# Kernel tuning notes

Hardware: AMD Instinct MI355X
Metric: run time of the kernel (lower is better)

The kernel has to match this reference:

```python
import jax, jax.numpy as jnp
import numpy as np

C = 1024
RANK = 8


def _layernorm(x, g, b, eps=1e-5):
    mu = jnp.mean(x, axis=-1, keepdims=True)
    var = jnp.var(x, axis=-1, keepdims=True)
    return (x - mu) * jax.lax.rsqrt(var + eps) * g + b


def setup_inputs() -> dict:
    key = jax.random.key(0)
    ks = jax.random.split(key, 10)
    B, T = 4, 4096
    x = jax.random.normal(ks[0], (B, T, C), dtype=jnp.float32)
    # parameters (match torch inits)
    W0 = jnp.eye(C, dtype=jnp.float32) * 0.1
    A_init = jax.random.normal(ks[1], (C, RANK), dtype=jnp.float32) * 0.01
    B_init = jnp.zeros((RANK, C), dtype=jnp.float32)
    log_lr = jnp.full((C,), float(np.log(0.1)), dtype=jnp.float32)
    s = 1.0 / np.sqrt(C)
    Wq = jax.random.uniform(ks[2], (C, C), minval=-s, maxval=s, dtype=jnp.float32)
    Wk = jax.random.uniform(ks[3], (C, C), minval=-s, maxval=s, dtype=jnp.float32)
    Wv = jax.random.uniform(ks[4], (C, C), minval=-s, maxval=s, dtype=jnp.float32)
    Wo = jax.random.uniform(ks[5], (C, C), minval=-s, maxval=s, dtype=jnp.float32)
    Wg = jax.random.uniform(ks[6], (C, C), minval=-s, maxval=s, dtype=jnp.float32)
    ln_g = jnp.ones((C,), dtype=jnp.float32)
    ln_b = jnp.zeros((C,), dtype=jnp.float32)
    ls_g = jnp.full((C,), 1e-4, dtype=jnp.float32)  # LayerScale gamma
    return {"x": x, "W0": W0, "A_init": A_init, "B_init": B_init,
            "log_lr": log_lr, "Wq": Wq, "Wk": Wk, "Wv": Wv, "Wo": Wo,
            "Wg": Wg, "ln_g": ln_g, "ln_b": ln_b, "ls_g": ls_g}


def reference(x, W0, A_init, B_init, log_lr, Wq, Wk, Wv, Wo, Wg, ln_g, ln_b, ls_g):
    B, T, _ = x.shape
    h = _layernorm(x, ln_g, ln_b)
    # dual-form TTT (training path: q/k/v projections, full K @ W0)
    Q = jnp.einsum('btc,dc->btd', h, Wq)
    K = jnp.einsum('btc,dc->btd', h, Wk)
    V = jnp.einsum('btc,dc->btd', h, Wv)
    lr = jnp.minimum(jnp.exp(log_lr), 1.0)  # clamp(max=1.0)
    y0 = jnp.einsum('btc,cd->btd', K, W0) + jnp.einsum('btr,rd->btd', jnp.einsum('btc,cr->btr', K, A_init), B_init)
    error = y0 - V
    loss = jnp.mean(error ** 2)
    gradient = K * error                     # [B,T,C]
    grad_cumsum = jnp.cumsum(gradient, axis=1)
    grad_shift = jnp.concatenate([jnp.zeros((B, 1, gradient.shape[-1]), gradient.dtype), grad_cumsum[:, :-1, :]], axis=1)
    correction = Q * lr[None, None, :] * grad_shift
    pos = jnp.arange(1, T + 1, dtype=correction.dtype)
    pos_scale = (1.0 / (1.0 + 0.1 * jnp.log(pos)))[None, :, None]
    out = y0 - correction * pos_scale
    # gate, out projection, layer scale, residual
    gate = jax.nn.sigmoid(jnp.einsum('btc,dc->btd', x, Wg))
    out = out * gate
    out = jnp.einsum('btc,dc->btd', out, Wo) * ls_g
    return (x + out, loss)
```

## Files before the change

### kernel.cpp

```cpp
#include <hip/hip_runtime.h>
#include <stdint.h>
#include <math.h>

typedef unsigned short u16;
typedef __attribute__((ext_vector_type(8))) short short8;
typedef __attribute__((ext_vector_type(4))) float f32x4;

__device__ __forceinline__ float bf2f(u16 u){
  union { unsigned int i; float f; } v; v.i = ((unsigned int)u) << 16; return v.f;
}
__device__ __forceinline__ u16 f2bf(float f){
  union { float f; unsigned int i; } v; v.f = f;
  return (u16)((v.i + 0x7FFFu + ((v.i >> 16) & 1u)) >> 16);
}

__global__ void ln_prep(const float* __restrict__ x, const float* __restrict__ g,
                        const float* __restrict__ bta, u16* __restrict__ h,
                        u16* __restrict__ xb, float* __restrict__ loss){
  if (blockIdx.x == 0 && threadIdx.x == 0) loss[0] = 0.f;
  int row = blockIdx.x, tid = threadIdx.x;
  const float4* xr = (const float4*)(x + (size_t)row * 1024);
  float4 v = xr[tid];
  float s  = v.x + v.y + v.z + v.w;
  float s2 = v.x*v.x + v.y*v.y + v.z*v.z + v.w*v.w;
  #pragma unroll
  for (int o = 32; o > 0; o >>= 1){ s += __shfl_down(s, o); s2 += __shfl_down(s2, o); }
  __shared__ float red[8];
  if ((tid & 63) == 0){ red[tid >> 6] = s; red[4 + (tid >> 6)] = s2; }
  __syncthreads();
  float ts = red[0]+red[1]+red[2]+red[3];
  float t2 = red[4]+red[5]+red[6]+red[7];
  float mu   = ts * (1.0f/1024.0f);
  float var  = t2 * (1.0f/1024.0f) - mu*mu;
  float rstd = rsqrtf(var + 1e-5f);
  float4 gg = ((const float4*)g)[tid];
  float4 bb = ((const float4*)bta)[tid];
  ushort4 hv, xv;
  hv.x = f2bf((v.x-mu)*rstd*gg.x + bb.x);
  hv.y = f2bf((v.y-mu)*rstd*gg.y + bb.y);
  hv.z = f2bf((v.z-mu)*rstd*gg.z + bb.z);
  hv.w = f2bf((v.w-mu)*rstd*gg.w + bb.w);
  xv.x = f2bf(v.x); xv.y = f2bf(v.y); xv.z = f2bf(v.z); xv.w = f2bf(v.w);
  ((ushort4*)h )[(size_t)row*256 + tid] = hv;
  ((ushort4*)xb)[(size_t)row*256 + tid] = xv;
}

__global__ void conv5(const float* __restrict__ a, const float* __restrict__ b,
                      const float* __restrict__ c, const float* __restrict__ d,
                      const float* __restrict__ e,
                      u16* oa, u16* ob, u16* oc, u16* od, u16* oe){
  int sel = blockIdx.y;
  const float* s = sel==0?a : sel==1?b : sel==2?c : sel==3?d : e;
  u16* o = sel==0?oa : sel==1?ob : sel==2?oc : sel==3?od : oe;
  int i = blockIdx.x*256 + threadIdx.x;
  float4 v = ((const float4*)s)[i];
  ushort4 r; r.x=f2bf(v.x); r.y=f2bf(v.y); r.z=f2bf(v.z); r.w=f2bf(v.w);
  ((ushort4*)o)[i] = r;
}

__global__ void weff_k(const float* __restrict__ W0, const float* __restrict__ Ai,
                       const float* __restrict__ Bi, u16* __restrict__ Wet){
  __shared__ float tile[32][33];
  int d0 = blockIdx.x*32, e0 = blockIdx.y*32;
  int tid = threadIdx.x;
  int lr = tid >> 5, lc = tid & 31;
  #pragma unroll
  for (int s = 0; s < 4; ++s){
    int e = e0 + s*8 + lr, d = d0 + lc;
    float v = W0[(size_t)e*1024 + d];
    #pragma unroll
    for (int r = 0; r < 8; ++r) v += Ai[e*8 + r] * Bi[(size_t)r*1024 + d];
    tile[s*8 + lr][lc] = v;
  }
  __syncthreads();
  #pragma unroll
  for (int s = 0; s < 4; ++s){
    int d = d0 + s*8 + lr, e = e0 + lc;
    Wet[(size_t)d*1024 + e] = f2bf(tile[lc][s*8 + lr]);
  }
}

template<int EPI>
__device__ __forceinline__ void gemm256_body(const u16* __restrict__ A, const u16* __restrict__ Bm,
    u16* __restrict__ Cb, float* __restrict__ Cf, const float* __restrict__ lsg,
    const float* __restrict__ xres, int mblk, int nblk)
{
  __shared__ u16 As[4][8192];
  __shared__ u16 Bs[4][8192];
  const int tid  = threadIdx.x;
  const int lane = tid & 63;
  const int w    = tid >> 6;
  const int wm = w >> 2, wn = w & 3;
  const int l15 = lane & 15, quad = lane >> 4;
  const int m0 = mblk * 256, n0 = nblk * 256;

  const int sl   = (lane & 7) ^ (lane >> 3);
  const int srow = 2*(w*8 + (lane >> 3)) + (sl >> 2);
  const int scol = (sl & 3) * 8;
  const u16* gA = A  + (size_t)(m0 + srow)*1024 + scol;
  const u16* gB = Bm + (size_t)(n0 + srow)*1024 + scol;
  const int ldsOff = w * 512;

  const int phys8 = (((((l15 & 1) << 2) | quad) ^ (l15 >> 1))) * 8;
  const int rdA = (wm*64 + (l15 >> 1))*64 + phys8;
  const int rdB = (wn*32 + (l15 >> 1))*64 + phys8;

  f32x4 acc[8][4] = {};

#define STAGE(T) do{ \
    const int _s = (T) & 3; \
    const size_t _k = (size_t)(T) * 32; \
    __builtin_amdgcn_global_load_lds((const __attribute__((address_space(1))) unsigned int*)(gA + _k), \
        (__attribute__((address_space(3))) unsigned int*)(&As[_s][ldsOff]), 16, 0, 0); \
    __builtin_amdgcn_global_load_lds((const __attribute__((address_space(1))) unsigned int*)(gA + _k + 131072), \
        (__attribute__((address_space(3))) unsigned int*)(&As[_s][ldsOff + 4096]), 16, 0, 0); \
    __builtin_amdgcn_global_load_lds((const __attribute__((address_space(1))) unsigned int*)(gB + _k), \
        (__attribute__((address_space(3))) unsigned int*)(&Bs[_s][ldsOff]), 16, 0, 0); \
    __builtin_amdgcn_global_load_lds((const __attribute__((address_space(1))) unsigned int*)(gB + _k + 131072), \
        (__attribute__((address_space(3))) unsigned int*)(&Bs[_s][ldsOff + 4096]), 16, 0, 0); \
  }while(0)

#define COMPUTE(T) do{ \
    const int _s = (T) & 3; \
    const u16* _as = &As[_s][0]; \
    const u16* _bs = &Bs[_s][0]; \
    short8 afv[8], bfv[4]; \
    _Pragma("unroll") \
    for (int _j = 0; _j < 4; ++_j) bfv[_j] = *(const short8*)(_bs + rdB + _j*512); \
    _Pragma("unroll") \
    for (int _i = 0; _i < 8; ++_i) afv[_i] = *(const short8*)(_as + rdA + _i*512); \
    __builtin_amdgcn_s_setprio(1); \
    _Pragma("unroll") \
    for (int _i = 0; _i < 8; ++_i){ \
      _Pragma("unroll") \
      for (int _j = 0; _j < 4; ++_j) \
        acc[_i][_j] = __builtin_amdgcn_mfma_f32_16x16x32_bf16(afv[_i], bfv[_j], acc[_i][_j], 0, 0, 0); \
    } \
    __builtin_amdgcn_s_setprio(0); \
  }while(0)

  STAGE(0); STAGE(1); STAGE(2);

  #pragma unroll 1
  for (int t = 0; t < 29; ++t){
    asm volatile("s_waitcnt vmcnt(8)" ::: "memory");
    __builtin_amdgcn_s_barrier();
    __builtin_amdgcn_sched_barrier(0);
    STAGE(t + 3);
    COMPUTE(t);
  }
  asm volatile("s_waitcnt vmcnt(8)" ::: "memory");
  __builtin_amdgcn_s_barrier();
  __builtin_amdgcn_sched_barrier(0);
  COMPUTE(29);
  asm volatile("s_waitcnt vmcnt(4)" ::: "memory");
  __builtin_amdgcn_s_barrier();
  __builtin_amdgcn_sched_barrier(0);
  COMPUTE(30);
  asm volatile("s_waitcnt vmcnt(0)" ::: "memory");
  __builtin_amdgcn_s_barrier();
  __builtin_amdgcn_sched_barrier(0);
  COMPUTE(31);
#undef STAGE
#undef COMPUTE

  const int rbase = quad * 4;
  if (EPI == 0){
    #pragma unroll
    for (int i = 0; i < 8; ++i){
      int row = m0 + wm*128 + i*16 + rbase;
      #pragma unroll
      for (int j = 0; j < 4; ++j){
        int col = n0 + wn*64 + j*16 + l15;
        #pragma unroll
        for (int r = 0; r < 4; ++r)
          Cb[(size_t)(row + r)*1024 + col] = f2bf(acc[i][j][r]);
      }
    }
  } else {
    float lsv[4];
    #pragma unroll
    for (int j = 0; j < 4; ++j) lsv[j] = lsg[n0 + wn*64 + j*16 + l15];
    #pragma unroll
    for (int i = 0; i < 8; ++i){
      int row = m0 + wm*128 + i*16 + rbase;
      #pragma unroll
      for (int j = 0; j < 4; ++j){
        int col = n0 + wn*64 + j*16 + l15;
        #pragma unroll
        for (int r = 0; r < 4; ++r){
          size_t idx = (size_t)(row + r)*1024 + col;
          Cf[idx] = acc[i][j][r] * lsv[j] + xres[idx];
        }
      }
    }
  }
}

__global__ __launch_bounds__(512, 2) void gemm_qkvg(
    const u16* __restrict__ h, const u16* __restrict__ xb,
    const u16* __restrict__ Wqb, const u16* __restrict__ Wkb,
    const u16* __restrict__ Wvb, const u16* __restrict__ Wgb,
    u16* __restrict__ Qb, u16* __restrict__ Kb,
    u16* __restrict__ Vb, u16* __restrict__ Gb){
  int bid = blockIdx.x;
  int swz = (bid & 7) * 128 + (bid >> 3);
  int mblk = swz >> 4;
  int rem  = swz & 15;
  int sel  = rem >> 2, nblk = rem & 3;
  const u16* A  = (sel == 3) ? xb : h;
  const u16* Bm = sel==0?Wqb : sel==1?Wkb : sel==2?Wvb : Wgb;
  u16* Out      = sel==0?Qb  : sel==1?Kb  : sel==2?Vb  : Gb;
  gemm256_body<0>(A, Bm, Out, nullptr, nullptr, nullptr, mblk, nblk);
}

__global__ __launch_bounds__(512, 2) void gemm_plain(
    const u16* __restrict__ A, const u16* __restrict__ Bm, u16* __restrict__ C){
  int bid = blockIdx.x;
  int swz = (bid & 7) * 32 + (bid >> 3);
  gemm256_body<0>(A, Bm, C, nullptr, nullptr, nullptr, swz >> 2, swz & 3);
}

__global__ __launch_bounds__(512, 2) void gemm_final(
    const u16* __restrict__ A, const u16* __restrict__ Bm,
    float* __restrict__ C, const float* __restrict__ lsg,
    const float* __restrict__ xres){
  int bid = blockIdx.x;
  int swz = (bid & 7) * 32 + (bid >> 3);
  gemm256_body<1>(A, Bm, nullptr, C, lsg, xres, swz >> 2, swz & 3);
}

__global__ void scan1(const u16* __restrict__ Kb, const u16* __restrict__ Vb,
                      const u16* __restrict__ Yb, float* __restrict__ part,
                      float* __restrict__ loss){
  int tid = threadIdx.x;
  int c = blockIdx.x*256 + tid;
  int ch = blockIdx.y, b = blockIdx.z;
  size_t base = ((size_t)b*4096 + (size_t)ch*128)*1024 + c;
  float g = 0.f, ls = 0.f;
  #pragma unroll 8
  for (int t = 0; t < 128; ++t){
    size_t idx = base + (size_t)t*1024;
    float kv = bf2f(Kb[idx]), vv = bf2f(Vb[idx]), yv = bf2f(Yb[idx]);
    float e = yv - vv;
    g += kv*e; ls += e*e;
  }
  part[((size_t)(b*32 + ch))*1024 + c] = g;
  #pragma unroll
  for (int o = 32; o > 0; o >>= 1) ls += __shfl_down(ls, o);
  __shared__ float red[4];
  if ((tid & 63) == 0) red[tid >> 6] = ls;
  __syncthreads();
  if (tid == 0) atomicAdd(loss, red[0]+red[1]+red[2]+red[3]);
}

__global__ void scan2(const u16* __restrict__ Kb, const u16* __restrict__ Vb,
                      const u16* __restrict__ Yb, const u16* __restrict__ Qb,
                      const u16* __restrict__ Gb, const float* __restrict__ part,
                      const float* __restrict__ llr, u16* __restrict__ OutPre){
  int tid = threadIdx.x;
  int c = blockIdx.x*256 + tid;
  int ch = blockIdx.y, b = blockIdx.z;
  float run = 0.f;
  for (int j = 0; j < ch; ++j) run += part[((size_t)(b*32 + j))*1024 + c];
  float lrc = fminf(expf(llr[c]), 1.0f);
  size_t base = ((size_t)b*4096 + (size_t)ch*128)*1024 + c;
  #pragma unroll 4
  for (int t = 0; t < 128; ++t){
    size_t idx = base + (size_t)t*1024;
    float kv = bf2f(Kb[idx]), vv = bf2f(Vb[idx]), yv = bf2f(Yb[idx]);
    float qv = bf2f(Qb[idx]), gl = bf2f(Gb[idx]);
    float e = yv - vv;
    int tg = ch*128 + t + 1;
    float ps = 1.0f/(1.0f + 0.1f*logf((float)tg));
    float gate = 1.0f/(1.0f + expf(-gl));
    float o = (yv - qv*lrc*run*ps) * gate;
    OutPre[idx] = f2bf(o);
    run += kv*e;
  }
}

__global__ void finloss(const float* __restrict__ loss, float* __restrict__ o){
  o[0] = loss[0] * (1.0f/16777216.0f);
}

extern "C" void kernel_launch(void* const* d_in, const int* in_sizes, int n_in,
                              void* d_out, int out_size, void* d_ws, size_t ws_size,
                              hipStream_t stream){
  const float* x   = (const float*)d_in[0];
  const float* W0  = (const float*)d_in[1];
  const float* Ai  = (const float*)d_in[2];
  const float* Bi  = (const float*)d_in[3];
  const float* llr = (const float*)d_in[4];
  const float* Wq  = (const float*)d_in[5];
  const float* Wk  = (const float*)d_in[6];
  const float* Wv  = (const float*)d_in[7];
  const float* Wo  = (const float*)d_in[8];
  const float* Wg  = (const float*)d_in[9];
  const float* lng = (const float*)d_in[10];
  const float* lnb = (const float*)d_in[11];
  const float* lsg = (const float*)d_in[12];
  float* out = (float*)d_out;

  const size_t TOK = 16384, CC = 1024;
  char* p = (char*)d_ws;
  float* loss = (float*)p; p += 256;
  u16* h   = (u16*)p; p += TOK*CC*2;
  u16* xb  = (u16*)p; p += TOK*CC*2;
  u16* Qb  = (u16*)p; p += TOK*CC*2;
  u16* Kb  = (u16*)p; p += TOK*CC*2;
  u16* Vb  = (u16*)p; p += TOK*CC*2;
  u16* Gb  = (u16*)p; p += TOK*CC*2;
  u16* Wqb = (u16*)p; p += CC*CC*2;
  u16* Wkb = (u16*)p; p += CC*CC*2;
  u16* Wvb = (u16*)p; p += CC*CC*2;
  u16* Wgb = (u16*)p; p += CC*CC*2;
  u16* Wob = (u16*)p; p += CC*CC*2;
  u16* Wet = (u16*)p; p += CC*CC*2;
  float* part = (float*)p; p += (size_t)4*32*1024*4;

  ln_prep<<<16384, 256, 0, stream>>>(x, lng, lnb, h, xb, loss);
  conv5<<<dim3(1024, 5), 256, 0, stream>>>(Wq, Wk, Wv, Wg, Wo, Wqb, Wkb, Wvb, Wgb, Wob);
  weff_k<<<dim3(32, 32), 256, 0, stream>>>(W0, Ai, Bi, Wet);
  gemm_qkvg<<<1024, 512, 0, stream>>>(h, xb, Wqb, Wkb, Wvb, Wgb, Qb, Kb, Vb, Gb);
  gemm_plain<<<256, 512, 0, stream>>>(Kb, Wet, h);
  scan1<<<dim3(4, 32, 4), 256, 0, stream>>>(Kb, Vb, h, part, loss);
  scan2<<<dim3(4, 32, 4), 256, 0, stream>>>(Kb, Vb, h, Qb, Gb, part, llr, Qb);
  gemm_final<<<256, 512, 0, stream>>>(Qb, Wob, out, lsg, x);
  finloss<<<1, 1, 0, stream>>>(loss, out + 16777216);
}
```

Measured before the change: 495.7 us.

## Split GEMM k-step into two half-slices interleaving global loads with MFMA

Restructures the 256x256 bf16 GEMM main loop so each k-step is split into two halves over the N fragments, issuing the A and B global-to-LDS prefetches separately between the halves, with extra barriers and lgkmcnt waits. It also unrolls the loop by four. The intent is finer-grained interleaving of memory issue, LDS reads and MFMA work, closer to a ping-pong style schedule. The extra barriers per k-step add synchronisation cost and could stall the waves.

```diff
diff --git a/kernel.cpp b/kernel.cpp
--- a/kernel.cpp
+++ b/kernel.cpp
@@ -80,6 +80,11 @@
   }
 }
 
+#define VMW(N)  asm volatile("s_waitcnt vmcnt(" #N ")" ::: "memory")
+#define LGKM0   asm volatile("s_waitcnt lgkmcnt(0)" ::: "memory")
+#define SBAR    __builtin_amdgcn_s_barrier()
+#define SCHED0  __builtin_amdgcn_sched_barrier(0)
+
 template<int EPI>
 __device__ __forceinline__ void gemm256_body(const u16* __restrict__ A, const u16* __restrict__ Bm,
     u16* __restrict__ Cb, float* __restrict__ Cf, const float* __restrict__ lsg,
@@ -107,62 +112,69 @@
 
   f32x4 acc[8][4] = {};
 
-#define STAGE(T) do{ \
-    const int _s = (T) & 3; \
-    const size_t _k = (size_t)(T) * 32; \
+#define SA(T) do{ const int _ss=(T)&3; const size_t _k=(size_t)(T)*32; \
     __builtin_amdgcn_global_load_lds((const __attribute__((address_space(1))) unsigned int*)(gA + _k), \
-        (__attribute__((address_space(3))) unsigned int*)(&As[_s][ldsOff]), 16, 0, 0); \
+        (__attribute__((address_space(3))) unsigned int*)(&As[_ss][ldsOff]), 16, 0, 0); \
     __builtin_amdgcn_global_load_lds((const __attribute__((address_space(1))) unsigned int*)(gA + _k + 131072), \
-        (__attribute__((address_space(3))) unsigned int*)(&As[_s][ldsOff + 4096]), 16, 0, 0); \
+        (__attribute__((address_space(3))) unsigned int*)(&As[_ss][ldsOff + 4096]), 16, 0, 0); \
+  }while(0)
+#define SB(T) do{ const int _ss=(T)&3; const size_t _k=(size_t)(T)*32; \
     __builtin_amdgcn_global_load_lds((const __attribute__((address_space(1))) unsigned int*)(gB + _k), \
-        (__attribute__((address_space(3))) unsigned int*)(&Bs[_s][ldsOff]), 16, 0, 0); \
+        (__attribute__((address_space(3))) unsigned int*)(&Bs[_ss][ldsOff]), 16, 0, 0); \
     __builtin_amdgcn_global_load_lds((const __attribute__((address_space(1))) unsigned int*)(gB + _k + 131072), \
-        (__attribute__((address_space(3))) unsigned int*)(&Bs[_s][ldsOff + 4096]), 16, 0, 0); \
+        (__attribute__((address_space(3))) unsigned int*)(&Bs[_ss][ldsOff + 4096]), 16, 0, 0); \
   }while(0)
 
-#define COMPUTE(T) do{ \
+#define SLICE(T, DS, VMOP) do{ \
     const int _s = (T) & 3; \
     const u16* _as = &As[_s][0]; \
     const u16* _bs = &Bs[_s][0]; \
     short8 afv[8], bfv[4]; \
-    _Pragma("unroll") \
-    for (int _j = 0; _j < 4; ++_j) bfv[_j] = *(const short8*)(_bs + rdB + _j*512); \
+    bfv[0] = *(const short8*)(_bs + rdB); \
+    bfv[1] = *(const short8*)(_bs + rdB + 512); \
     _Pragma("unroll") \
     for (int _i = 0; _i < 8; ++_i) afv[_i] = *(const short8*)(_as + rdA + _i*512); \
+    if (DS) SA((T)+3); \
+    SBAR; LGKM0; SCHED0; \
     __builtin_amdgcn_s_setprio(1); \
     _Pragma("unroll") \
     for (int _i = 0; _i < 8; ++_i){ \
-      _Pragma("unroll") \
-      for (int _j = 0; _j < 4; ++_j) \
-        acc[_i][_j] = __builtin_amdgcn_mfma_f32_16x16x32_bf16(afv[_i], bfv[_j], acc[_i][_j], 0, 0, 0); \
+      acc[_i][0] = __builtin_amdgcn_mfma_f32_16x16x32_bf16(afv[_i], bfv[0], acc[_i][0], 0, 0, 0); \
+      acc[_i][1] = __builtin_amdgcn_mfma_f32_16x16x32_bf16(afv[_i], bfv[1], acc[_i][1], 0, 0, 0); \
     } \
-    __builtin_amdgcn_s_setprio(0); \
+    __builtin_amdgcn_s_setprio(0); SCHED0; SBAR; \
+    bfv[2] = *(const short8*)(_bs + rdB + 1024); \
+    bfv[3] = *(const short8*)(_bs + rdB + 1536); \
+    if (DS) SB((T)+3); \
+    VMOP; \
+    SBAR; LGKM0; SCHED0; \
+    __builtin_amdgcn_s_setprio(1); \
+    _Pragma("unroll") \
+    for (int _i = 0; _i < 8; ++_i){ \
+      acc[_i][2] = __builtin_amdgcn_mfma_f32_16x16x32_bf16(afv[_i], bfv[2], acc[_i][2], 0, 0, 0); \
+      acc[_i][3] = __builtin_amdgcn_mfma_f32_16x16x32_bf16(afv[_i], bfv[3], acc[_i][3], 0, 0, 0); \
+    } \
+    __builtin_amdgcn_s_setprio(0); SCHED0; SBAR; \
   }while(0)
 
-  STAGE(0); STAGE(1); STAGE(2);
+  SA(0); SB(0); SA(1); SB(1); SA(2); SB(2);
+  VMW(8);
+  SBAR;
 
   #pragma unroll 1
-  for (int t = 0; t < 29; ++t){
-    asm volatile("s_waitcnt vmcnt(8)" ::: "memory");
-    __builtin_amdgcn_s_barrier();
-    __builtin_amdgcn_sched_barrier(0);
-    STAGE(t + 3);
-    COMPUTE(t);
-  }
-  asm volatile("s_waitcnt vmcnt(8)" ::: "memory");
-  __builtin_amdgcn_s_barrier();
-  __builtin_amdgcn_sched_barrier(0);
-  COMPUTE(29);
-  asm volatile("s_waitcnt vmcnt(4)" ::: "memory");
-  __builtin_amdgcn_s_barrier();
-  __builtin_amdgcn_sched_barrier(0);
-  COMPUTE(30);
-  asm volatile("s_waitcnt vmcnt(0)" ::: "memory");
-  __builtin_amdgcn_s_barrier();
-  __builtin_amdgcn_sched_barrier(0);
-  COMPUTE(31);
-#undef STAGE
-#undef COMPUTE
+  for (int t = 0; t < 28; t += 4){
+    SLICE(t+0, 1, VMW(8));
+    SLICE(t+1, 1, VMW(8));
+    SLICE(t+2, 1, VMW(8));
+    SLICE(t+3, 1, VMW(8));
+  }
+  SLICE(28, 1, VMW(8));
+  SLICE(29, 0, VMW(4));
+  SLICE(30, 0, VMW(0));
+  SLICE(31, 0, (void)0);
+#undef SLICE
+#undef SA
+#undef SB
 
   const int rbase = quad * 4;
   if (EPI == 0){
```

Result: faster. 458.1 us (-7.6%).
